# Kernel tuning notes

Hardware: AMD Instinct MI355X
Metric: run time of the kernel (lower is better)

## Reference

```python
import jax, jax.numpy as jnp
import numpy as np

D, L, DIM, G = 64, 64, 512, 256      # dialogues, utterances/dialogue, feat dim, graph dim
TOPK_FRAC = 0.2
TAU = 0.07


def setup_inputs() -> dict:
    key = jax.random.key(0)
    ks = jax.random.split(key, 7)
    N = D * L
    t = jax.random.normal(ks[0], (N, DIM), dtype=jnp.float32)
    a = jax.random.normal(ks[1], (N, DIM), dtype=jnp.float32)
    v = jax.random.normal(ks[2], (N, DIM), dtype=jnp.float32)
    W_fc = jax.random.normal(ks[3], (DIM, G), dtype=jnp.float32) / np.sqrt(DIM)
    b_fc = jnp.zeros((G,), dtype=jnp.float32)
    W_h = jax.random.normal(ks[4], (G, G), dtype=jnp.float32) / np.sqrt(G)
    b_h = jnp.zeros((G,), dtype=jnp.float32)
    dia_len = np.full((D,), L, dtype=np.int64)  # uniform dialogue lengths
    return {"t": t, "a": a, "v": v, "W_fc": W_fc, "b_fc": b_fc,
            "W_h": W_h, "b_h": b_h, "dia_len": dia_len}


def _contrastive_loss(x, y, tau=TAU):
    # symmetric InfoNCE with matched-index positives
    xn = x / (jnp.linalg.norm(x, axis=-1, keepdims=True) + 1e-8)
    yn = y / (jnp.linalg.norm(y, axis=-1, keepdims=True) + 1e-8)
    sim = (xn @ yn.T) / tau                     # [N, N]
    pos_xy = jnp.diagonal(jax.nn.log_softmax(sim, axis=1))
    pos_yx = jnp.diagonal(jax.nn.log_softmax(sim, axis=0))
    return -(pos_xy.mean() + pos_yx.mean()) / 2.0


def _forward(t, a, v, W_fc, b_fc, W_h, b_h, dia_len):
    dl = np.asarray(dia_len)
    d, l = dl.shape[0], int(dl[0])              # uniform lengths assumed
    m = 3 * l                                   # nodes (and hyperedges) per dialogue
    k = int(l * TOPK_FRAC)
    dim = t.shape[-1]

    # per-dialogue node features in original order [t_i; a_i; v_i]
    feat = jnp.concatenate([t.reshape(d, l, dim),
                            a.reshape(d, l, dim),
                            v.reshape(d, l, dim)], axis=1)   # [d, m, dim]

    # squared euclidean distances (same ordering as torch.cdist for top-k smallest)
    sq = jnp.sum(feat * feat, axis=-1)                        # [d, m]
    d2 = sq[:, :, None] + sq[:, None, :] - 2.0 * jnp.einsum('dmf,dnf->dmn', feat, feat)
    d2 = jax.lax.stop_gradient(jnp.maximum(d2, 0.0))
    _, idx = jax.lax.top_k(-d2, k)                            # [d, m, k] nearest nodes

    # boolean incidence H[d, e, n] = node n participates in hyperedge e
    # (set-union dedup in the original == boolean OR here)
    node_ids = jnp.arange(m)
    H_nb = (idx[..., None] == node_ids).any(axis=2)           # [d, m, m]
    u = node_ids // 3                                         # central utterance of edge j
    cent = ((node_ids[None, :] == u[:, None]) |
            (node_ids[None, :] == u[:, None] + l) |
            (node_ids[None, :] == u[:, None] + 2 * l))        # [m, m]
    H = (H_nb | cent[None]).astype(feat.dtype)                # [d, m, m]

    # fc projection
    X = feat @ W_fc + b_fc                                    # [d, m, G]

    # hypergraph conv: node -> hyperedge (mean) -> node (mean), then Linear+ReLU
    deg_e = H.sum(axis=2, keepdims=True)                      # [d, m, 1]
    E = jnp.einsum('den,dng->deg', H, X) / deg_e              # edge features
    deg_v = H.sum(axis=1)[..., None]                          # [d, m, 1]
    Y = jnp.einsum('den,deg->dng', H, E) / deg_v              # node features
    out = jax.nn.relu(Y @ W_h + b_h)                          # [d, m, G]

    # reverse_features: regroup by modality across dialogues
    tn = out[:, :l].reshape(d * l, -1)
    an = out[:, l:2 * l].reshape(d * l, -1)
    vn = out[:, 2 * l:].reshape(d * l, -1)
    out_cat = jnp.concatenate([tn, an, vn], axis=1)           # [N, 3G]

    loss = (_contrastive_loss(tn, an) + _contrastive_loss(tn, vn)
            + _contrastive_loss(an, vn)) / 3.0
    return out_cat, loss


def reference(t, a, v, W_fc, b_fc, W_h, b_h, dia_len):
    return _forward(t, a, v, W_fc, b_fc, W_h, b_h, dia_len)
```

## Files before the change

kernel.cpp:

```cpp
#include <hip/hip_runtime.h>
#include <math.h>

#define NDIAL 64
#define M3    192
#define DIMF  512
#define GDIM  256
#define NROW  4096
#define TOPK  12
#define INV_TAU (1.0f/0.07f)

typedef __attribute__((ext_vector_type(8))) short bf16x8;
typedef __attribute__((ext_vector_type(4))) float f32x4;
typedef __attribute__((ext_vector_type(8))) ushort us8;
typedef _Float16 f16x8 __attribute__((ext_vector_type(8)));
typedef _Float16 f16x4v __attribute__((ext_vector_type(4)));
typedef __attribute__((address_space(3))) ushort lds_us;
typedef const __attribute__((address_space(1))) ushort gm_us;

__device__ __forceinline__ ushort f2bf(float f) {
    unsigned u = __float_as_uint(f);
    unsigned r = (u + 0x7fff + ((u >> 16) & 1)) >> 16;
    return (ushort)r;
}

template<int KDIM>
__device__ __forceinline__ void mm64bt(
    const float* __restrict__ A, int lda,
    const float* __restrict__ B, int ldb,
    float acc[4][4])
{
    __shared__ float As[64][33];
    __shared__ float Bs[32][68];
    const int tid = threadIdx.x;
    const int tx = tid & 15, ty = tid >> 4;

#pragma unroll
    for (int r = 0; r < 4; r++)
#pragma unroll
        for (int c = 0; c < 4; c++) acc[r][c] = 0.f;

    for (int k0 = 0; k0 < KDIM; k0 += 32) {
#pragma unroll
        for (int i = 0; i < 2; i++) {
            int f = tid + i * 256;
            int m = f >> 3, k4 = f & 7;
            const float4 v4 = *(const float4*)(A + (size_t)m * lda + k0 + k4 * 4);
            As[m][k4 * 4 + 0] = v4.x;
            As[m][k4 * 4 + 1] = v4.y;
            As[m][k4 * 4 + 2] = v4.z;
            As[m][k4 * 4 + 3] = v4.w;
        }
#pragma unroll
        for (int i = 0; i < 2; i++) {
            int f = tid + i * 256;
            int n = f >> 3, k4 = f & 7;
            const float4 v4 = *(const float4*)(B + (size_t)n * ldb + k0 + k4 * 4);
            Bs[k4 * 4 + 0][n] = v4.x;
            Bs[k4 * 4 + 1][n] = v4.y;
            Bs[k4 * 4 + 2][n] = v4.z;
            Bs[k4 * 4 + 3][n] = v4.w;
        }
        __syncthreads();
#pragma unroll
        for (int kk = 0; kk < 32; kk++) {
            float4 b = *(const float4*)&Bs[kk][tx * 4];
#pragma unroll
            for (int r = 0; r < 4; r++) {
                float av = As[ty * 4 + r][kk];
                acc[r][0] += av * b.x;
                acc[r][1] += av * b.y;
                acc[r][2] += av * b.z;
                acc[r][3] += av * b.w;
            }
        }
        __syncthreads();
    }
}

template<int KD, int NW>
__device__ __forceinline__ void hgemm_bt(const _Float16* __restrict__ A, int lda,
                                         const _Float16* __restrict__ B, int ldb,
                                         f32x4 acc[4][4]) {
    __shared__ __align__(16) _Float16 As[64 * 40];
    __shared__ __align__(16) _Float16 Bs[NW * 64 * 40];
    const int tid = threadIdx.x;
    const int lane = tid & 63, w = tid >> 6;
    const int qd = lane >> 4, l15 = lane & 15;

#pragma unroll
    for (int fm = 0; fm < 4; fm++)
#pragma unroll
        for (int fn = 0; fn < 4; fn++)
            acc[fm][fn] = (f32x4){0.f, 0.f, 0.f, 0.f};

    for (int k0 = 0; k0 < KD; k0 += 32) {
        for (int f = tid; f < 256; f += NW * 64) {
            int row = f >> 2, c8 = f & 3;
            *(float4*)&As[row * 40 + c8 * 8] =
                *(const float4*)&A[(size_t)row * lda + k0 + c8 * 8];
        }
#pragma unroll
        for (int i = 0; i < 4; i++) {
            int f = tid + i * NW * 64;
            int row = f >> 2, c8 = f & 3;
            *(float4*)&Bs[row * 40 + c8 * 8] =
                *(const float4*)&B[(size_t)row * ldb + k0 + c8 * 8];
        }
        __syncthreads();
        f16x8 af[4], bfr[4];
#pragma unroll
        for (int fm = 0; fm < 4; fm++)
            af[fm] = *(const f16x8*)&As[(fm * 16 + l15) * 40 + qd * 8];
#pragma unroll
        for (int fn = 0; fn < 4; fn++)
            bfr[fn] = *(const f16x8*)&Bs[(w * 64 + fn * 16 + l15) * 40 + qd * 8];
#pragma unroll
        for (int fm = 0; fm < 4; fm++)
#pragma unroll
            for (int fn = 0; fn < 4; fn++)
                acc[fm][fn] = __builtin_amdgcn_mfma_f32_16x16x32_f16(
                    af[fm], bfr[fn], acc[fm][fn], 0, 0, 0);
        __syncthreads();
    }
}

__device__ __forceinline__ const float* node_ptr(const float* t, const float* a,
                                                 const float* v, int d, int j) {
    int mod = j >> 6, i = j & 63;
    const float* base = (mod == 0) ? t : (mod == 1) ? a : v;
    return base + (size_t)(d * 64 + i) * DIMF;
}

__global__ void kprep(const float* __restrict__ t, const float* __restrict__ a,
                      const float* __restrict__ v, const float* __restrict__ Wfc,
                      const float* __restrict__ Wh, _Float16* __restrict__ featb,
                      _Float16* __restrict__ WfcT, _Float16* __restrict__ WhT,
                      float* __restrict__ sq, float* __restrict__ rs,
                      float* __restrict__ cs, float* __restrict__ degV,
                      _Float16* __restrict__ HbT) {
    int b = blockIdx.x, tid = threadIdx.x;
    if (b < 6144) {
        int e = (b * 256 + tid) * 4;
        int d = e / (M3 * DIMF);
        int rem = e % (M3 * DIMF);
        int n = rem / DIMF, kk = rem % DIMF;
        int mod = n >> 6, i = n & 63;
        const float* src = ((mod == 0) ? t : (mod == 1) ? a : v)
                           + (size_t)(d * 64 + i) * DIMF + kk;
        float4 x = *(const float4*)src;
        f16x4v o = {(_Float16)x.x, (_Float16)x.y, (_Float16)x.z, (_Float16)x.w};
        *(f16x4v*)&featb[e] = o;
    } else if (b < 6272) {
        int e = ((b - 6144) * 256 + tid) * 4;
        int g = e >> 9, kk = e & 511;
        f16x4v o = {(_Float16)Wfc[(size_t)(kk + 0) * GDIM + g],
                    (_Float16)Wfc[(size_t)(kk + 1) * GDIM + g],
                    (_Float16)Wfc[(size_t)(kk + 2) * GDIM + g],
                    (_Float16)Wfc[(size_t)(kk + 3) * GDIM + g]};
        *(f16x4v*)&WfcT[(size_t)g * DIMF + kk] = o;
    } else if (b < 6336) {
        int e = ((b - 6272) * 256 + tid) * 4;
        int go = e >> 8, g = e & 255;
        f16x4v o = {(_Float16)Wh[(size_t)(g + 0) * GDIM + go],
                    (_Float16)Wh[(size_t)(g + 1) * GDIM + go],
                    (_Float16)Wh[(size_t)(g + 2) * GDIM + go],
                    (_Float16)Wh[(size_t)(g + 3) * GDIM + go]};
        *(f16x4v*)&WhT[(size_t)go * GDIM + g] = o;
    } else if (b < 9408) {
        int lane = tid & 63, wv = tid >> 6;
        int n = (b - 6336) * 4 + wv;
        int d = n / M3, j = n % M3;
        const float4* s4 = (const float4*)node_ptr(t, a, v, d, j);
        float s = 0.f;
#pragma unroll
        for (int q = 0; q < 2; q++) {
            float4 x = s4[lane + q * 64];
            s += x.x * x.x + x.y * x.y + x.z * x.z + x.w * x.w;
        }
        for (int o = 32; o; o >>= 1) s += __shfl_down(s, o);
        if (lane == 0) sq[n] = s;
    } else if (b < 9456) {
        int i = (b - 9408) * 256 + tid;
        rs[i] = 0.f; cs[i] = 0.f; degV[i] = 0.f;
    } else {
        int i = (b - 9456) * 256 + tid;
        ulonglong2 z = {0ull, 0ull};
        *(ulonglong2*)&HbT[(size_t)i * 8] = z;
    }
}

__global__ void k1_d2(const float* __restrict__ t, const float* __restrict__ a,
                      const float* __restrict__ v, const float* __restrict__ sq,
                      float* __restrict__ d2) {
    int tileid = blockIdx.x;
    int d = blockIdx.y;
    int bi = (tileid < 3) ? 0 : (tileid < 5) ? 1 : 2;
    int bj = (tileid < 3) ? tileid : (tileid < 5) ? tileid - 2 : 2;
    const float* A = ((bi == 0) ? t : (bi == 1) ? a : v) + (size_t)d * 64 * DIMF;
    const float* B = ((bj == 0) ? t : (bj == 1) ? a : v) + (size_t)d * 64 * DIMF;
    float acc[4][4];
    mm64bt<DIMF>(A, DIMF, B, DIMF, acc);
    int tx = threadIdx.x & 15, ty = threadIdx.x >> 4;
    const float* sqd = sq + d * M3;
    float* outp = d2 + (size_t)d * M3 * M3;
#pragma unroll
    for (int r = 0; r < 4; r++)
#pragma unroll
        for (int c = 0; c < 4; c++) {
            int il = bi * 64 + ty * 4 + r;
            int jl = bj * 64 + tx * 4 + c;
            float vv = fmaxf(sqd[il] + sqd[jl] - 2.f * acc[r][c], 0.f);
            outp[(size_t)il * M3 + jl] = vv;
            if (bi != bj) outp[(size_t)jl * M3 + il] = vv;
        }
}

__global__ void k2_topk(const float* __restrict__ d2, _Float16* __restrict__ Hb,
                        _Float16* __restrict__ HbT, float* __restrict__ degE,
                        float* __restrict__ degV) {
    int lane = threadIdx.x & 63, wv = threadIdx.x >> 6;
    int r = blockIdx.x * 4 + wv;
    int d = r / M3, e = r % M3;
    const float* row = d2 + (size_t)r * M3;
    float w0 = row[lane], w1 = row[lane + 64], w2 = row[lane + 128];
    bool s0 = false, s1 = false, s2 = false;
#pragma unroll
    for (int it = 0; it < TOPK; it++) {
        float bv = w0; int bi = lane;
        if (w1 < bv) { bv = w1; bi = lane + 64; }
        if (w2 < bv) { bv = w2; bi = lane + 128; }
#pragma unroll
        for (int o = 1; o < 64; o <<= 1) {
            float ov = __shfl_xor(bv, o);
            int   oi = __shfl_xor(bi, o);
            if (ov < bv || (ov == bv && oi < bi)) { bv = ov; bi = oi; }
        }
        if (bi == lane)            { s0 = true; w0 = 3.4e38f; }
        else if (bi == lane + 64)  { s1 = true; w1 = 3.4e38f; }
        else if (bi == lane + 128) { s2 = true; w2 = 3.4e38f; }
    }
    int u = e / 3;
    if (lane == u) { s0 = true; s1 = true; s2 = true; }
    float f0 = s0 ? 1.f : 0.f, f1 = s1 ? 1.f : 0.f, f2 = s2 ? 1.f : 0.f;
    _Float16* Hrow = Hb + (size_t)r * M3;
    Hrow[lane] = (_Float16)f0;
    Hrow[lane + 64] = (_Float16)f1;
    Hrow[lane + 128] = (_Float16)f2;
    float cnt = f0 + f1 + f2;
#pragma unroll
    for (int o = 1; o < 64; o <<= 1) cnt += __shfl_xor(cnt, o);
    if (lane == 0) degE[r] = cnt;
    float* dv = degV + d * M3;
    _Float16* HT = HbT + (size_t)d * M3 * M3;
    if (s0) { atomicAdd(&dv[lane], 1.f);       HT[(size_t)lane * M3 + e] = (_Float16)1.f; }
    if (s1) { atomicAdd(&dv[lane + 64], 1.f);  HT[(size_t)(lane + 64) * M3 + e] = (_Float16)1.f; }
    if (s2) { atomicAdd(&dv[lane + 128], 1.f); HT[(size_t)(lane + 128) * M3 + e] = (_Float16)1.f; }
}

__global__ void k3_x(const _Float16* __restrict__ WfcT, const _Float16* __restrict__ featb,
                     const float* __restrict__ bfc, _Float16* __restrict__ XT) {
    int gb = blockIdx.x, d = blockIdx.y;
    const _Float16* A = WfcT + (size_t)gb * 64 * DIMF;
    const _Float16* B = featb + (size_t)d * M3 * DIMF;
    f32x4 acc[4][4];
    hgemm_bt<DIMF, 3>(A, DIMF, B, DIMF, acc);
    int lane = threadIdx.x & 63, w = threadIdx.x >> 6;
    int qd = lane >> 4, l15 = lane & 15;
    _Float16* out = XT + (size_t)d * GDIM * M3;
#pragma unroll
    for (int fm = 0; fm < 4; fm++)
#pragma unroll
        for (int rg = 0; rg < 4; rg++) {
            int g = gb * 64 + fm * 16 + qd * 4 + rg;
            float bias = bfc[g];
#pragma unroll
            for (int fn = 0; fn < 4; fn++) {
                int n = w * 64 + fn * 16 + l15;
                out[(size_t)g * M3 + n] = (_Float16)(acc[fm][fn][rg] + bias);
            }
        }
}

__global__ void k4_E(const _Float16* __restrict__ XT, const _Float16* __restrict__ Hb,
                     const float* __restrict__ degE, _Float16* __restrict__ ET) {
    int gb = blockIdx.x, d = blockIdx.y;
    const _Float16* A = XT + (size_t)d * GDIM * M3 + (size_t)gb * 64 * M3;
    const _Float16* B = Hb + (size_t)d * M3 * M3;
    f32x4 acc[4][4];
    hgemm_bt<M3, 3>(A, M3, B, M3, acc);
    int lane = threadIdx.x & 63, w = threadIdx.x >> 6;
    int qd = lane >> 4, l15 = lane & 15;
    float ide[4];
#pragma unroll
    for (int fn = 0; fn < 4; fn++)
        ide[fn] = 1.f / degE[d * M3 + w * 64 + fn * 16 + l15];
    _Float16* out = ET + (size_t)d * GDIM * M3;
#pragma unroll
    for (int fm = 0; fm < 4; fm++)
#pragma unroll
        for (int rg = 0; rg < 4; rg++) {
            int g = gb * 64 + fm * 16 + qd * 4 + rg;
#pragma unroll
            for (int fn = 0; fn < 4; fn++) {
                int e = w * 64 + fn * 16 + l15;
                out[(size_t)g * M3 + e] = (_Float16)(acc[fm][fn][rg] * ide[fn]);
            }
        }
}

__global__ void k5_Y(const _Float16* __restrict__ HbT, const _Float16* __restrict__ ET,
                     const float* __restrict__ degV, _Float16* __restrict__ Y) {
    int nb = blockIdx.x, d = blockIdx.y;
    const _Float16* A = HbT + (size_t)d * M3 * M3 + (size_t)nb * 64 * M3;
    const _Float16* B = ET + (size_t)d * GDIM * M3;
    f32x4 acc[4][4];
    hgemm_bt<M3, 4>(A, M3, B, M3, acc);
    int lane = threadIdx.x & 63, w = threadIdx.x >> 6;
    int qd = lane >> 4, l15 = lane & 15;
    _Float16* out = Y + ((size_t)d * M3 + nb * 64) * GDIM;
#pragma unroll
    for (int fm = 0; fm < 4; fm++)
#pragma unroll
        for (int rg = 0; rg < 4; rg++) {
            int ml = fm * 16 + qd * 4 + rg;
            float idv = 1.f / degV[d * M3 + nb * 64 + ml];
#pragma unroll
            for (int fn = 0; fn < 4; fn++) {
                int g = w * 64 + fn * 16 + l15;
                out[(size_t)ml * GDIM + g] = (_Float16)(acc[fm][fn][rg] * idv);
            }
        }
}

__global__ __launch_bounds__(256) void k6_out(const _Float16* __restrict__ Y,
                                              const _Float16* __restrict__ WhT,
                                              const float* __restrict__ bh,
                                              float* __restrict__ outp,
                                              ushort* __restrict__ xnb) {
    __shared__ float tile[64 * 256];
    __shared__ float ssq[64];
    int b = blockIdx.x, tid = threadIdx.x;
    if (tid < 64) ssq[tid] = 0.f;
    const _Float16* A = Y + (size_t)b * 64 * GDIM;
    f32x4 acc[4][4];
    hgemm_bt<GDIM, 4>(A, GDIM, WhT, GDIM, acc);
    int lane = tid & 63, w = tid >> 6;
    int qd = lane >> 4, l15 = lane & 15;
    int d = b / 3, mod = b % 3;
    float bb[4];
#pragma unroll
    for (int fn = 0; fn < 4; fn++)
        bb[fn] = bh[w * 64 + fn * 16 + l15];
#pragma unroll
    for (int fm = 0; fm < 4; fm++)
#pragma unroll
        for (int rg = 0; rg < 4; rg++) {
            int i = fm * 16 + qd * 4 + rg;
            float* orow = outp + (size_t)(d * 64 + i) * 768 + mod * GDIM;
            float s2 = 0.f;
#pragma unroll
            for (int fn = 0; fn < 4; fn++) {
                int go = w * 64 + fn * 16 + l15;
                float vv = fmaxf(acc[fm][fn][rg] + bb[fn], 0.f);
                orow[go] = vv;
                tile[i * 256 + go] = vv;
                s2 += vv * vv;
            }
            s2 += __shfl_xor(s2, 1);
            s2 += __shfl_xor(s2, 2);
            s2 += __shfl_xor(s2, 4);
            s2 += __shfl_xor(s2, 8);
            if (l15 == 0) atomicAdd(&ssq[i], s2);
        }
    __syncthreads();
    if (tid < 64) ssq[tid] = 1.f / (sqrtf(ssq[tid]) + 1e-8f);
    __syncthreads();
#pragma unroll
    for (int it = 0; it < 8; it++) {
        int f = tid + it * 256;
        int row = f >> 5, c = f & 31;
        float4 xa = *(const float4*)&tile[row * 256 + c * 8];
        float4 xb = *(const float4*)&tile[row * 256 + c * 8 + 4];
        float iv = ssq[row];
        us8 o = {f2bf(xa.x * iv), f2bf(xa.y * iv), f2bf(xa.z * iv), f2bf(xa.w * iv),
                 f2bf(xb.x * iv), f2bf(xb.y * iv), f2bf(xb.z * iv), f2bf(xb.w * iv)};
        int rx = d * 64 + row;
        int slot = (c & 24) | ((c & 7) ^ (row & 7));
        *(us8*)&xnb[((size_t)mod * NROW + rx) * GDIM + slot * 8] = o;
    }
}

#define TILE2 256
__global__ __launch_bounds__(512, 2) void k9_mfma(const ushort* __restrict__ xnb,
                                                  float* __restrict__ rs,
                                                  float* __restrict__ cs,
                                                  float* __restrict__ diag) {
    int cj = blockIdx.x, ci = blockIdx.y, p = blockIdx.z;
    int px = (p == 2) ? 1 : 0;
    int py = (p == 0) ? 1 : 2;
    const ushort* A = xnb + ((size_t)px * NROW + ci * TILE2) * GDIM;
    const ushort* B = xnb + ((size_t)py * NROW + cj * TILE2) * GDIM;

    __shared__ __align__(16) ushort As[TILE2 * 64];
    __shared__ __align__(16) ushort Bs[TILE2 * 64];

    const int tid = threadIdx.x;
    const int lane = tid & 63, w = tid >> 6;
    const int wrow = w >> 2, wcol = w & 3;
    const int qd = lane >> 4, l15 = lane & 15;
    const int lrow = lane >> 3, lslot = lane & 7;

    f32x4 acc[8][4] = {};

    for (int kh = 0; kh < 4; kh++) {
#pragma unroll
        for (int j = 0; j < 4; j++) {
            int rr = w * 32 + j * 8 + lrow;
            __builtin_amdgcn_global_load_lds(
                (gm_us*)(A + (size_t)rr * GDIM + kh * 64 + lslot * 8),
                (lds_us*)&As[(w * 32 + j * 8) * 64], 16, 0, 0);
            __builtin_amdgcn_global_load_lds(
                (gm_us*)(B + (size_t)rr * GDIM + kh * 64 + lslot * 8),
                (lds_us*)&Bs[(w * 32 + j * 8) * 64], 16, 0, 0);
        }
        __syncthreads();
#pragma unroll
        for (int kk = 0; kk < 2; kk++) {
            bf16x8 af[8], bfv[4];
#pragma unroll
            for (int fm = 0; fm < 8; fm++) {
                int ar = wrow * 128 + fm * 16 + l15;
                af[fm] = *(const bf16x8*)&As[ar * 64 + ((kk * 4 + qd) ^ (ar & 7)) * 8];
            }
#pragma unroll
            for (int fn = 0; fn < 4; fn++) {
                int br = wcol * 64 + fn * 16 + l15;
                bfv[fn] = *(const bf16x8*)&Bs[br * 64 + ((kk * 4 + qd) ^ (br & 7)) * 8];
            }
#pragma unroll
            for (int fm = 0; fm < 8; fm++)
#pragma unroll
                for (int fn = 0; fn < 4; fn++)
                    acc[fm][fn] = __builtin_amdgcn_mfma_f32_16x16x32_bf16(
                        af[fm], bfv[fn], acc[fm][fn], 0, 0, 0);
        }
        __syncthreads();
    }

    float rloc[8][4] = {};
    float cloc[4] = {};
#pragma unroll
    for (int fm = 0; fm < 8; fm++)
#pragma unroll
        for (int fn = 0; fn < 4; fn++)
#pragma unroll
            for (int rg = 0; rg < 4; rg++) {
                float s = acc[fm][fn][rg] * INV_TAU;
                float e = __expf(s);
                rloc[fm][rg] += e;
                cloc[fn] += e;
                int grow = ci * TILE2 + wrow * 128 + fm * 16 + qd * 4 + rg;
                int gcol = cj * TILE2 + wcol * 64 + fn * 16 + l15;
                if (grow == gcol) diag[p * NROW + grow] = s;
            }
#pragma unroll
    for (int fm = 0; fm < 8; fm++)
#pragma unroll
        for (int rg = 0; rg < 4; rg++) {
            float s = rloc[fm][rg];
            s += __shfl_xor(s, 1);
            s += __shfl_xor(s, 2);
            s += __shfl_xor(s, 4);
            s += __shfl_xor(s, 8);
            if (l15 == 0)
                atomicAdd(&rs[p * NROW + ci * TILE2 + wrow * 128 + fm * 16 + qd * 4 + rg], s);
        }
#pragma unroll
    for (int fn = 0; fn < 4; fn++) {
        float s = cloc[fn];
        s += __shfl_xor(s, 16);
        s += __shfl_xor(s, 32);
        if (qd == 0)
            atomicAdd(&cs[p * NROW + cj * TILE2 + wcol * 64 + fn * 16 + l15], s);
    }
}

__global__ void k10_loss(const float* __restrict__ diag, const float* __restrict__ rs,
                         const float* __restrict__ cs, float* __restrict__ outp) {
    float acc = 0.f;
    for (int i = threadIdx.x; i < 3 * NROW; i += 256)
        acc += 2.f * diag[i] - logf(rs[i]) - logf(cs[i]);
    int lane = threadIdx.x & 63, wv = threadIdx.x >> 6;
    for (int o = 32; o; o >>= 1) acc += __shfl_down(acc, o);
    __shared__ float red[4];
    if (lane == 0) red[wv] = acc;
    __syncthreads();
    if (threadIdx.x == 0) {
        float tot = red[0] + red[1] + red[2] + red[3];
        outp[(size_t)NROW * 768] = -tot / (NROW * 6.0f);
    }
}

extern "C" void kernel_launch(void* const* d_in, const int* in_sizes, int n_in,
                              void* d_out, int out_size, void* d_ws, size_t ws_size,
                              hipStream_t stream) {
    const float* t   = (const float*)d_in[0];
    const float* a   = (const float*)d_in[1];
    const float* v   = (const float*)d_in[2];
    const float* Wfc = (const float*)d_in[3];
    const float* bfc = (const float*)d_in[4];
    const float* Wh  = (const float*)d_in[5];
    const float* bh  = (const float*)d_in[6];
    float* outp = (float*)d_out;
    float* ws = (float*)d_ws;

    float* sq    = ws;
    float* d2    = sq + 12288;
    float* HbF   = d2 + 2359296;
    float* HbTF  = HbF + 1179648;
    float* degE  = HbTF + 1179648;
    float* degV  = degE + 12288;
    float* featF = degV + 12288;
    float* WfcTF = featF + 3145728;
    float* WhTF  = WfcTF + 65536;
    float* XTF   = WhTF + 32768;
    float* ETF   = XTF + 1572864;
    float* YF    = ETF + 1572864;
    float* rs    = YF + 1572864;
    float* cs    = rs + 12288;
    float* diag  = cs + 12288;

    _Float16* Hb    = (_Float16*)HbF;
    _Float16* HbT   = (_Float16*)HbTF;
    _Float16* featb = (_Float16*)featF;
    _Float16* WfcT  = (_Float16*)WfcTF;
    _Float16* WhT   = (_Float16*)WhTF;
    _Float16* XT    = (_Float16*)XTF;
    _Float16* ET    = (_Float16*)ETF;
    _Float16* Y     = (_Float16*)YF;
    ushort*   xnb   = (ushort*)d2;

    kprep  <<<10608, 256, 0, stream>>>(t, a, v, Wfc, Wh, featb, WfcT, WhT,
                                       sq, rs, cs, degV, HbT);
    k1_d2  <<<dim3(6, 64), 256, 0, stream>>>(t, a, v, sq, d2);
    k2_topk<<<3072, 256, 0, stream>>>(d2, Hb, HbT, degE, degV);
    k3_x   <<<dim3(4, 64), 192, 0, stream>>>(WfcT, featb, bfc, XT);
    k4_E   <<<dim3(4, 64), 192, 0, stream>>>(XT, Hb, degE, ET);
    k5_Y   <<<dim3(3, 64), 256, 0, stream>>>(HbT, ET, degV, Y);
    k6_out <<<192, 256, 0, stream>>>(Y, WhT, bh, outp, xnb);
    k9_mfma<<<dim3(16, 16, 3), 512, 0, stream>>>(xnb, rs, cs, diag);
    k10_loss<<<1, 256, 0, stream>>>(diag, rs, cs, outp);
}
```

Before: 288.9 us.

## Reassociate hypergraph pipeline and use split-fp16 MFMA for distances

Replaces the fp32 SIMT distance GEMM with an MFMA GEMM on hi/lo fp16 splits of the features (three products per tile) to keep near-fp32 accuracy. Reassociates the hypergraph conv: precomputes W_fc·W_h and a fused bias, forms the node-to-node matrix H^T·diag(1/deg_e)·H per dialogue, applies it to the raw transposed features, and then does one GEMM against the fused weight. This removes the separate fc-projection, edge and node kernels and the X/E/Y intermediates, but adds a wider K=512 final GEMM, extra feature copies (hi, lo, transposed) and fp16 rounding of the fused weights and aggregated features.

```diff
diff --git a/kernel.cpp b/kernel.cpp
--- a/kernel.cpp
+++ b/kernel.cpp
@@ -21,60 +21,6 @@
     unsigned u = __float_as_uint(f);
     unsigned r = (u + 0x7fff + ((u >> 16) & 1)) >> 16;
     return (ushort)r;
-}
-
-template<int KDIM>
-__device__ __forceinline__ void mm64bt(
-    const float* __restrict__ A, int lda,
-    const float* __restrict__ B, int ldb,
-    float acc[4][4])
-{
-    __shared__ float As[64][33];
-    __shared__ float Bs[32][68];
-    const int tid = threadIdx.x;
-    const int tx = tid & 15, ty = tid >> 4;
-
-#pragma unroll
-    for (int r = 0; r < 4; r++)
-#pragma unroll
-        for (int c = 0; c < 4; c++) acc[r][c] = 0.f;
-
-    for (int k0 = 0; k0 < KDIM; k0 += 32) {
-#pragma unroll
-        for (int i = 0; i < 2; i++) {
-            int f = tid + i * 256;
-            int m = f >> 3, k4 = f & 7;
-            const float4 v4 = *(const float4*)(A + (size_t)m * lda + k0 + k4 * 4);
-            As[m][k4 * 4 + 0] = v4.x;
-            As[m][k4 * 4 + 1] = v4.y;
-            As[m][k4 * 4 + 2] = v4.z;
-            As[m][k4 * 4 + 3] = v4.w;
-        }
-#pragma unroll
-        for (int i = 0; i < 2; i++) {
-            int f = tid + i * 256;
-            int n = f >> 3, k4 = f & 7;
-            const float4 v4 = *(const float4*)(B + (size_t)n * ldb + k0 + k4 * 4);
-            Bs[k4 * 4 + 0][n] = v4.x;
-            Bs[k4 * 4 + 1][n] = v4.y;
-            Bs[k4 * 4 + 2][n] = v4.z;
-            Bs[k4 * 4 + 3][n] = v4.w;
-        }
-        __syncthreads();
-#pragma unroll
-        for (int kk = 0; kk < 32; kk++) {
-            float4 b = *(const float4*)&Bs[kk][tx * 4];
-#pragma unroll
-            for (int r = 0; r < 4; r++) {
-                float av = As[ty * 4 + r][kk];
-                acc[r][0] += av * b.x;
-                acc[r][1] += av * b.y;
-                acc[r][2] += av * b.z;
-                acc[r][3] += av * b.w;
-            }
-        }
-        __syncthreads();
-    }
 }
 
 template<int KD, int NW>
@@ -133,8 +79,9 @@
 
 __global__ void kprep(const float* __restrict__ t, const float* __restrict__ a,
                       const float* __restrict__ v, const float* __restrict__ Wfc,
-                      const float* __restrict__ Wh, _Float16* __restrict__ featb,
-                      _Float16* __restrict__ WfcT, _Float16* __restrict__ WhT,
+                      const float* __restrict__ Wh, _Float16* __restrict__ feath,
+                      _Float16* __restrict__ featl, _Float16* __restrict__ featT,
+                      _Float16* __restrict__ Wfch, _Float16* __restrict__ WhT,
                       float* __restrict__ sq, float* __restrict__ rs,
                       float* __restrict__ cs, float* __restrict__ degV,
                       _Float16* __restrict__ HbT) {
@@ -148,16 +95,16 @@
         const float* src = ((mod == 0) ? t : (mod == 1) ? a : v)
                            + (size_t)(d * 64 + i) * DIMF + kk;
         float4 x = *(const float4*)src;
-        f16x4v o = {(_Float16)x.x, (_Float16)x.y, (_Float16)x.z, (_Float16)x.w};
-        *(f16x4v*)&featb[e] = o;
+        f16x4v h = {(_Float16)x.x, (_Float16)x.y, (_Float16)x.z, (_Float16)x.w};
+        f16x4v l = {(_Float16)(x.x - (float)h.x), (_Float16)(x.y - (float)h.y),
+                    (_Float16)(x.z - (float)h.z), (_Float16)(x.w - (float)h.w)};
+        *(f16x4v*)&feath[e] = h;
+        *(f16x4v*)&featl[e] = l;
     } else if (b < 6272) {
         int e = ((b - 6144) * 256 + tid) * 4;
-        int g = e >> 9, kk = e & 511;
-        f16x4v o = {(_Float16)Wfc[(size_t)(kk + 0) * GDIM + g],
-                    (_Float16)Wfc[(size_t)(kk + 1) * GDIM + g],
-                    (_Float16)Wfc[(size_t)(kk + 2) * GDIM + g],
-                    (_Float16)Wfc[(size_t)(kk + 3) * GDIM + g]};
-        *(f16x4v*)&WfcT[(size_t)g * DIMF + kk] = o;
+        float4 x = *(const float4*)&Wfc[e];
+        f16x4v o = {(_Float16)x.x, (_Float16)x.y, (_Float16)x.z, (_Float16)x.w};
+        *(f16x4v*)&Wfch[e] = o;
     } else if (b < 6336) {
         int e = ((b - 6272) * 256 + tid) * 4;
         int go = e >> 8, g = e & 255;
@@ -182,42 +129,145 @@
     } else if (b < 9456) {
         int i = (b - 9408) * 256 + tid;
         rs[i] = 0.f; cs[i] = 0.f; degV[i] = 0.f;
-    } else {
+    } else if (b < 11760) {
         int i = (b - 9456) * 256 + tid;
         ulonglong2 z = {0ull, 0ull};
         *(ulonglong2*)&HbT[(size_t)i * 8] = z;
-    }
-}
-
-__global__ void k1_d2(const float* __restrict__ t, const float* __restrict__ a,
-                      const float* __restrict__ v, const float* __restrict__ sq,
-                      float* __restrict__ d2) {
-    int tileid = blockIdx.x;
-    int d = blockIdx.y;
-    int bi = (tileid < 3) ? 0 : (tileid < 5) ? 1 : 2;
-    int bj = (tileid < 3) ? tileid : (tileid < 5) ? tileid - 2 : 2;
-    const float* A = ((bi == 0) ? t : (bi == 1) ? a : v) + (size_t)d * 64 * DIMF;
-    const float* B = ((bj == 0) ? t : (bj == 1) ? a : v) + (size_t)d * 64 * DIMF;
-    float acc[4][4];
-    mm64bt<DIMF>(A, DIMF, B, DIMF, acc);
-    int tx = threadIdx.x & 15, ty = threadIdx.x >> 4;
+    } else {
+        __shared__ _Float16 tl[64 * 72];
+        int idx = b - 11760;
+        int d = idx / 24, rem = idx % 24;
+        int jb = rem / 8, fb = rem % 8;
+        const float* src = ((jb == 0) ? t : (jb == 1) ? a : v)
+                           + (size_t)(d * 64) * DIMF + fb * 64;
+#pragma unroll
+        for (int it = 0; it < 4; it++) {
+            int jj = (tid >> 4) + it * 16, ff = (tid & 15) * 4;
+            float4 x = *(const float4*)&src[(size_t)jj * DIMF + ff];
+            tl[jj * 72 + ff + 0] = (_Float16)x.x;
+            tl[jj * 72 + ff + 1] = (_Float16)x.y;
+            tl[jj * 72 + ff + 2] = (_Float16)x.z;
+            tl[jj * 72 + ff + 3] = (_Float16)x.w;
+        }
+        __syncthreads();
+        _Float16* dst = featT + (size_t)d * DIMF * M3 + (size_t)(fb * 64) * M3 + jb * 64;
+#pragma unroll
+        for (int it = 0; it < 4; it++) {
+            int fr = (tid >> 4) + it * 16, jc = (tid & 15) * 4;
+            f16x4v o = {tl[(jc + 0) * 72 + fr], tl[(jc + 1) * 72 + fr],
+                        tl[(jc + 2) * 72 + fr], tl[(jc + 3) * 72 + fr]};
+            *(f16x4v*)&dst[(size_t)fr * M3 + jc] = o;
+        }
+    }
+}
+
+__global__ void kW(const _Float16* __restrict__ WhT, const _Float16* __restrict__ Wfch,
+                   const float* __restrict__ bfc, const float* __restrict__ bh,
+                   const float* __restrict__ Wh, _Float16* __restrict__ W2t,
+                   float* __restrict__ b2) {
+    if (blockIdx.x == 8) {
+        int go = threadIdx.x;
+        float s = bh[go];
+        for (int g = 0; g < GDIM; g++) s += bfc[g] * Wh[(size_t)g * GDIM + go];
+        b2[go] = s;
+        return;
+    }
+    int rb = blockIdx.x >> 1, cb = blockIdx.x & 1;
+    f32x4 acc[4][4];
+    hgemm_bt<GDIM, 4>(WhT + (size_t)rb * 64 * GDIM, GDIM,
+                      Wfch + (size_t)cb * 256 * GDIM, GDIM, acc);
+    int lane = threadIdx.x & 63, w = threadIdx.x >> 6;
+    int qd = lane >> 4, l15 = lane & 15;
+#pragma unroll
+    for (int fm = 0; fm < 4; fm++)
+#pragma unroll
+        for (int rg = 0; rg < 4; rg++) {
+            int go = rb * 64 + fm * 16 + qd * 4 + rg;
+#pragma unroll
+            for (int fn = 0; fn < 4; fn++) {
+                int f = cb * 256 + w * 64 + fn * 16 + l15;
+                W2t[(size_t)go * DIMF + f] = (_Float16)acc[fm][fn][rg];
+            }
+        }
+}
+
+__global__ __launch_bounds__(192) void k1_d2(const _Float16* __restrict__ feath,
+                                             const _Float16* __restrict__ featl,
+                                             const float* __restrict__ sq,
+                                             float* __restrict__ d2) {
+    __shared__ __align__(16) _Float16 Ah[64 * 40], Al[64 * 40];
+    __shared__ __align__(16) _Float16 Bh[M3 * 40], Bl[M3 * 40];
+    int rb = blockIdx.x, d = blockIdx.y;
+    const _Float16* ah = feath + ((size_t)d * M3 + rb * 64) * DIMF;
+    const _Float16* al = featl + ((size_t)d * M3 + rb * 64) * DIMF;
+    const _Float16* bh = feath + (size_t)d * M3 * DIMF;
+    const _Float16* bl = featl + (size_t)d * M3 * DIMF;
+    const int tid = threadIdx.x;
+    const int lane = tid & 63, w = tid >> 6;
+    const int qd = lane >> 4, l15 = lane & 15;
+
+    f32x4 acc[4][4] = {};
+    for (int k0 = 0; k0 < DIMF; k0 += 32) {
+        for (int f = tid; f < 256; f += 192) {
+            int row = f >> 2, c8 = f & 3;
+            *(float4*)&Ah[row * 40 + c8 * 8] =
+                *(const float4*)&ah[(size_t)row * DIMF + k0 + c8 * 8];
+            *(float4*)&Al[row * 40 + c8 * 8] =
+                *(const float4*)&al[(size_t)row * DIMF + k0 + c8 * 8];
+        }
+#pragma unroll
+        for (int i = 0; i < 4; i++) {
+            int f = tid + i * 192;
+            int row = f >> 2, c8 = f & 3;
+            *(float4*)&Bh[row * 40 + c8 * 8] =
+                *(const float4*)&bh[(size_t)row * DIMF + k0 + c8 * 8];
+            *(float4*)&Bl[row * 40 + c8 * 8] =
+                *(const float4*)&bl[(size_t)row * DIMF + k0 + c8 * 8];
+        }
+        __syncthreads();
+        f16x8 afh[4], afl[4], bfh[4], bfl[4];
+#pragma unroll
+        for (int fm = 0; fm < 4; fm++) {
+            afh[fm] = *(const f16x8*)&Ah[(fm * 16 + l15) * 40 + qd * 8];
+            afl[fm] = *(const f16x8*)&Al[(fm * 16 + l15) * 40 + qd * 8];
+        }
+#pragma unroll
+        for (int fn = 0; fn < 4; fn++) {
+            bfh[fn] = *(const f16x8*)&Bh[(w * 64 + fn * 16 + l15) * 40 + qd * 8];
+            bfl[fn] = *(const f16x8*)&Bl[(w * 64 + fn * 16 + l15) * 40 + qd * 8];
+        }
+#pragma unroll
+        for (int fm = 0; fm < 4; fm++)
+#pragma unroll
+            for (int fn = 0; fn < 4; fn++) {
+                acc[fm][fn] = __builtin_amdgcn_mfma_f32_16x16x32_f16(
+                    afh[fm], bfh[fn], acc[fm][fn], 0, 0, 0);
+                acc[fm][fn] = __builtin_amdgcn_mfma_f32_16x16x32_f16(
+                    afh[fm], bfl[fn], acc[fm][fn], 0, 0, 0);
+                acc[fm][fn] = __builtin_amdgcn_mfma_f32_16x16x32_f16(
+                    afl[fm], bfh[fn], acc[fm][fn], 0, 0, 0);
+            }
+        __syncthreads();
+    }
     const float* sqd = sq + d * M3;
     float* outp = d2 + (size_t)d * M3 * M3;
 #pragma unroll
-    for (int r = 0; r < 4; r++)
-#pragma unroll
-        for (int c = 0; c < 4; c++) {
-            int il = bi * 64 + ty * 4 + r;
-            int jl = bj * 64 + tx * 4 + c;
-            float vv = fmaxf(sqd[il] + sqd[jl] - 2.f * acc[r][c], 0.f);
-            outp[(size_t)il * M3 + jl] = vv;
-            if (bi != bj) outp[(size_t)jl * M3 + il] = vv;
-        }
-}
-
-__global__ void k2_topk(const float* __restrict__ d2, _Float16* __restrict__ Hb,
-                        _Float16* __restrict__ HbT, float* __restrict__ degE,
-                        float* __restrict__ degV) {
+    for (int fm = 0; fm < 4; fm++)
+#pragma unroll
+        for (int rg = 0; rg < 4; rg++) {
+            int il = rb * 64 + fm * 16 + qd * 4 + rg;
+            float si = sqd[il];
+#pragma unroll
+            for (int fn = 0; fn < 4; fn++) {
+                int jl = w * 64 + fn * 16 + l15;
+                outp[(size_t)il * M3 + jl] =
+                    fmaxf(si + sqd[jl] - 2.f * acc[fm][fn][rg], 0.f);
+            }
+        }
+}
+
+__global__ void k2_topk(const float* __restrict__ d2, _Float16* __restrict__ HbT,
+                        _Float16* __restrict__ HbTd, float* __restrict__ degV) {
     int lane = threadIdx.x & 63, wv = threadIdx.x >> 6;
     int r = blockIdx.x * 4 + wv;
     int d = r / M3, e = r % M3;
@@ -241,116 +291,88 @@
     }
     int u = e / 3;
     if (lane == u) { s0 = true; s1 = true; s2 = true; }
-    float f0 = s0 ? 1.f : 0.f, f1 = s1 ? 1.f : 0.f, f2 = s2 ? 1.f : 0.f;
-    _Float16* Hrow = Hb + (size_t)r * M3;
-    Hrow[lane] = (_Float16)f0;
-    Hrow[lane + 64] = (_Float16)f1;
-    Hrow[lane + 128] = (_Float16)f2;
-    float cnt = f0 + f1 + f2;
+    float cnt = (s0 ? 1.f : 0.f) + (s1 ? 1.f : 0.f) + (s2 ? 1.f : 0.f);
 #pragma unroll
     for (int o = 1; o < 64; o <<= 1) cnt += __shfl_xor(cnt, o);
-    if (lane == 0) degE[r] = cnt;
+    _Float16 rde = (_Float16)(1.f / cnt);
     float* dv = degV + d * M3;
-    _Float16* HT = HbT + (size_t)d * M3 * M3;
-    if (s0) { atomicAdd(&dv[lane], 1.f);       HT[(size_t)lane * M3 + e] = (_Float16)1.f; }
-    if (s1) { atomicAdd(&dv[lane + 64], 1.f);  HT[(size_t)(lane + 64) * M3 + e] = (_Float16)1.f; }
-    if (s2) { atomicAdd(&dv[lane + 128], 1.f); HT[(size_t)(lane + 128) * M3 + e] = (_Float16)1.f; }
-}
-
-__global__ void k3_x(const _Float16* __restrict__ WfcT, const _Float16* __restrict__ featb,
-                     const float* __restrict__ bfc, _Float16* __restrict__ XT) {
-    int gb = blockIdx.x, d = blockIdx.y;
-    const _Float16* A = WfcT + (size_t)gb * 64 * DIMF;
-    const _Float16* B = featb + (size_t)d * M3 * DIMF;
+    _Float16* HT  = HbT  + (size_t)d * M3 * M3;
+    _Float16* HTd = HbTd + (size_t)d * M3 * M3;
+    if (s0) { atomicAdd(&dv[lane], 1.f);
+              HT[(size_t)lane * M3 + e] = (_Float16)1.f;
+              HTd[(size_t)lane * M3 + e] = rde; }
+    if (s1) { atomicAdd(&dv[lane + 64], 1.f);
+              HT[(size_t)(lane + 64) * M3 + e] = (_Float16)1.f;
+              HTd[(size_t)(lane + 64) * M3 + e] = rde; }
+    if (s2) { atomicAdd(&dv[lane + 128], 1.f);
+              HT[(size_t)(lane + 128) * M3 + e] = (_Float16)1.f;
+              HTd[(size_t)(lane + 128) * M3 + e] = rde; }
+}
+
+__global__ __launch_bounds__(192) void kM(const _Float16* __restrict__ HbT,
+                                          const _Float16* __restrict__ HbTd,
+                                          _Float16* __restrict__ S) {
+    int rb = blockIdx.x, d = blockIdx.y;
     f32x4 acc[4][4];
-    hgemm_bt<DIMF, 3>(A, DIMF, B, DIMF, acc);
+    hgemm_bt<M3, 3>(HbT + (size_t)d * M3 * M3 + (size_t)rb * 64 * M3, M3,
+                    HbTd + (size_t)d * M3 * M3, M3, acc);
     int lane = threadIdx.x & 63, w = threadIdx.x >> 6;
     int qd = lane >> 4, l15 = lane & 15;
-    _Float16* out = XT + (size_t)d * GDIM * M3;
+    _Float16* out = S + (size_t)d * M3 * M3;
 #pragma unroll
     for (int fm = 0; fm < 4; fm++)
 #pragma unroll
         for (int rg = 0; rg < 4; rg++) {
-            int g = gb * 64 + fm * 16 + qd * 4 + rg;
-            float bias = bfc[g];
-#pragma unroll
-            for (int fn = 0; fn < 4; fn++) {
-                int n = w * 64 + fn * 16 + l15;
-                out[(size_t)g * M3 + n] = (_Float16)(acc[fm][fn][rg] + bias);
-            }
-        }
-}
-
-__global__ void k4_E(const _Float16* __restrict__ XT, const _Float16* __restrict__ Hb,
-                     const float* __restrict__ degE, _Float16* __restrict__ ET) {
-    int gb = blockIdx.x, d = blockIdx.y;
-    const _Float16* A = XT + (size_t)d * GDIM * M3 + (size_t)gb * 64 * M3;
-    const _Float16* B = Hb + (size_t)d * M3 * M3;
+            int i = rb * 64 + fm * 16 + qd * 4 + rg;
+#pragma unroll
+            for (int fn = 0; fn < 4; fn++) {
+                int j = w * 64 + fn * 16 + l15;
+                out[(size_t)i * M3 + j] = (_Float16)acc[fm][fn][rg];
+            }
+        }
+}
+
+__global__ void kZ(const _Float16* __restrict__ S, const _Float16* __restrict__ featT,
+                   const float* __restrict__ degV, _Float16* __restrict__ Z) {
+    int rb = blockIdx.x % 3, cb = blockIdx.x / 3, d = blockIdx.y;
     f32x4 acc[4][4];
-    hgemm_bt<M3, 3>(A, M3, B, M3, acc);
+    hgemm_bt<M3, 4>(S + (size_t)d * M3 * M3 + (size_t)rb * 64 * M3, M3,
+                    featT + (size_t)d * DIMF * M3 + (size_t)cb * 256 * M3, M3, acc);
     int lane = threadIdx.x & 63, w = threadIdx.x >> 6;
     int qd = lane >> 4, l15 = lane & 15;
-    float ide[4];
-#pragma unroll
-    for (int fn = 0; fn < 4; fn++)
-        ide[fn] = 1.f / degE[d * M3 + w * 64 + fn * 16 + l15];
-    _Float16* out = ET + (size_t)d * GDIM * M3;
 #pragma unroll
     for (int fm = 0; fm < 4; fm++)
 #pragma unroll
         for (int rg = 0; rg < 4; rg++) {
-            int g = gb * 64 + fm * 16 + qd * 4 + rg;
-#pragma unroll
-            for (int fn = 0; fn < 4; fn++) {
-                int e = w * 64 + fn * 16 + l15;
-                out[(size_t)g * M3 + e] = (_Float16)(acc[fm][fn][rg] * ide[fn]);
-            }
-        }
-}
-
-__global__ void k5_Y(const _Float16* __restrict__ HbT, const _Float16* __restrict__ ET,
-                     const float* __restrict__ degV, _Float16* __restrict__ Y) {
-    int nb = blockIdx.x, d = blockIdx.y;
-    const _Float16* A = HbT + (size_t)d * M3 * M3 + (size_t)nb * 64 * M3;
-    const _Float16* B = ET + (size_t)d * GDIM * M3;
-    f32x4 acc[4][4];
-    hgemm_bt<M3, 4>(A, M3, B, M3, acc);
-    int lane = threadIdx.x & 63, w = threadIdx.x >> 6;
-    int qd = lane >> 4, l15 = lane & 15;
-    _Float16* out = Y + ((size_t)d * M3 + nb * 64) * GDIM;
-#pragma unroll
-    for (int fm = 0; fm < 4; fm++)
-#pragma unroll
-        for (int rg = 0; rg < 4; rg++) {
-            int ml = fm * 16 + qd * 4 + rg;
-            float idv = 1.f / degV[d * M3 + nb * 64 + ml];
-#pragma unroll
-            for (int fn = 0; fn < 4; fn++) {
-                int g = w * 64 + fn * 16 + l15;
-                out[(size_t)ml * GDIM + g] = (_Float16)(acc[fm][fn][rg] * idv);
-            }
-        }
-}
-
-__global__ __launch_bounds__(256) void k6_out(const _Float16* __restrict__ Y,
-                                              const _Float16* __restrict__ WhT,
-                                              const float* __restrict__ bh,
-                                              float* __restrict__ outp,
-                                              ushort* __restrict__ xnb) {
+            int node = rb * 64 + fm * 16 + qd * 4 + rg;
+            float idv = 1.f / degV[d * M3 + node];
+            _Float16* zr = Z + ((size_t)d * M3 + node) * DIMF + cb * 256;
+#pragma unroll
+            for (int fn = 0; fn < 4; fn++) {
+                int f = w * 64 + fn * 16 + l15;
+                zr[f] = (_Float16)(acc[fm][fn][rg] * idv);
+            }
+        }
+}
+
+__global__ __launch_bounds__(256) void kO(const _Float16* __restrict__ Z,
+                                          const _Float16* __restrict__ W2t,
+                                          const float* __restrict__ b2,
+                                          float* __restrict__ outp,
+                                          ushort* __restrict__ xnb) {
     __shared__ float tile[64 * 256];
     __shared__ float ssq[64];
     int b = blockIdx.x, tid = threadIdx.x;
     if (tid < 64) ssq[tid] = 0.f;
-    const _Float16* A = Y + (size_t)b * 64 * GDIM;
     f32x4 acc[4][4];
-    hgemm_bt<GDIM, 4>(A, GDIM, WhT, GDIM, acc);
+    hgemm_bt<DIMF, 4>(Z + (size_t)b * 64 * DIMF, DIMF, W2t, DIMF, acc);
     int lane = tid & 63, w = tid >> 6;
     int qd = lane >> 4, l15 = lane & 15;
     int d = b / 3, mod = b % 3;
     float bb[4];
 #pragma unroll
     for (int fn = 0; fn < 4; fn++)
-        bb[fn] = bh[w * 64 + fn * 16 + l15];
+        bb[fn] = b2[w * 64 + fn * 16 + l15];
 #pragma unroll
     for (int fm = 0; fm < 4; fm++)
 #pragma unroll
@@ -515,39 +537,41 @@
     float* ws = (float*)d_ws;
 
     float* sq    = ws;
-    float* d2    = sq + 12288;
-    float* HbF   = d2 + 2359296;
-    float* HbTF  = HbF + 1179648;
-    float* degE  = HbTF + 1179648;
-    float* degV  = degE + 12288;
-    float* featF = degV + 12288;
-    float* WfcTF = featF + 3145728;
-    float* WhTF  = WfcTF + 65536;
-    float* XTF   = WhTF + 32768;
-    float* ETF   = XTF + 1572864;
-    float* YF    = ETF + 1572864;
-    float* rs    = YF + 1572864;
+    float* d2F   = sq + 12288;
+    float* HbTF  = d2F + 2359296;
+    float* HbTdF = HbTF + 1179648;
+    float* degV  = HbTdF + 1179648;
+    float* feathF= degV + 12288;
+    float* featlF= feathF + 3145728;
+    float* featTF= featlF + 3145728;
+    float* WfchF = featTF + 3145728;
+    float* WhTF  = WfchF + 65536;
+    float* W2tF  = WhTF + 32768;
+    float* b2    = W2tF + 65536;
+    float* rs    = b2 + 256;
     float* cs    = rs + 12288;
     float* diag  = cs + 12288;
 
-    _Float16* Hb    = (_Float16*)HbF;
     _Float16* HbT   = (_Float16*)HbTF;
-    _Float16* featb = (_Float16*)featF;
-    _Float16* WfcT  = (_Float16*)WfcTF;
+    _Float16* HbTd  = (_Float16*)HbTdF;
+    _Float16* feath = (_Float16*)feathF;
+    _Float16* featl = (_Float16*)featlF;
+    _Float16* featT = (_Float16*)featTF;
+    _Float16* Wfch  = (_Float16*)WfchF;
     _Float16* WhT   = (_Float16*)WhTF;
-    _Float16* XT    = (_Float16*)XTF;
-    _Float16* ET    = (_Float16*)ETF;
-    _Float16* Y     = (_Float16*)YF;
-    ushort*   xnb   = (ushort*)d2;
-
-    kprep  <<<10608, 256, 0, stream>>>(t, a, v, Wfc, Wh, featb, WfcT, WhT,
-                                       sq, rs, cs, degV, HbT);
-    k1_d2  <<<dim3(6, 64), 256, 0, stream>>>(t, a, v, sq, d2);
-    k2_topk<<<3072, 256, 0, stream>>>(d2, Hb, HbT, degE, degV);
-    k3_x   <<<dim3(4, 64), 192, 0, stream>>>(WfcT, featb, bfc, XT);
-    k4_E   <<<dim3(4, 64), 192, 0, stream>>>(XT, Hb, degE, ET);
-    k5_Y   <<<dim3(3, 64), 256, 0, stream>>>(HbT, ET, degV, Y);
-    k6_out <<<192, 256, 0, stream>>>(Y, WhT, bh, outp, xnb);
+    _Float16* W2t   = (_Float16*)W2tF;
+    _Float16* S     = (_Float16*)featlF;
+    _Float16* Z     = (_Float16*)feathF;
+    ushort*   xnb   = (ushort*)d2F;
+
+    kprep  <<<13296, 256, 0, stream>>>(t, a, v, Wfc, Wh, feath, featl, featT,
+                                       Wfch, WhT, sq, rs, cs, degV, HbT);
+    kW     <<<9, 256, 0, stream>>>(WhT, Wfch, bfc, bh, Wh, W2t, b2);
+    k1_d2  <<<dim3(3, 64), 192, 0, stream>>>(feath, featl, sq, d2F);
+    k2_topk<<<3072, 256, 0, stream>>>(d2F, HbT, HbTd, degV);
+    kM     <<<dim3(3, 64), 192, 0, stream>>>(HbT, HbTd, S);
+    kZ     <<<dim3(6, 64), 256, 0, stream>>>(S, featT, degV, Z);
+    kO     <<<192, 256, 0, stream>>>(Z, W2t, b2, outp, xnb);
     k9_mfma<<<dim3(16, 16, 3), 512, 0, stream>>>(xnb, rs, cs, diag);
     k10_loss<<<1, 256, 0, stream>>>(diag, rs, cs, outp);
 }
```

After: 290.3 us. No clear change (+0.5%).
